# Kernel optimization log

Measured on AMD Instinct MI355X. Metric: run time of the kernel, lower is better.

Reference implementation:

```python
import jax, jax.numpy as jnp
import numpy as np

H = 8          # num heads
HD = 64        # head dim
DV = 512       # values_dim
DC = 128       # coords_dim
DI = 512       # att_inner_dim
DF = 2048      # mlp inner dim


def _ln(x, g, b, eps=1e-5):
    mu = jnp.mean(x, -1, keepdims=True)
    var = jnp.mean((x - mu) ** 2, -1, keepdims=True)
    return (x - mu) * jax.lax.rsqrt(var + eps) * g + b


def _rms(x, g, eps=1e-6):
    return x * jax.lax.rsqrt(jnp.mean(x * x, -1, keepdims=True) + eps) * g


def _heads(x):  # b n (h d) -> b h n d
    b, n, _ = x.shape
    return x.reshape(b, n, H, HD).transpose(0, 2, 1, 3)


def setup_inputs() -> dict:
    key = jax.random.key(0)
    ks = iter(jax.random.split(key, 40))
    r = lambda shape, s=0.02: jax.random.normal(next(ks), shape, jnp.float32) * s
    inp = {
        'coords': jax.random.normal(next(ks), (4, 4096, DC), jnp.float32),
        'values': jax.random.normal(next(ks), (4, 4096, DV), jnp.float32),
        'Lv': jax.random.normal(next(ks), (4, 1024, DV), jnp.float32),
        'Lc': jax.random.normal(next(ks), (4, 1024, DC), jnp.float32),
        'lam': jax.random.normal(next(ks), (1,), jnp.float32),
        'lvn_g': jnp.ones((DV,)), 'lvn_b': jnp.zeros((DV,)),
        'lcn_g': jnp.ones((DC,)), 'lcn_b': jnp.zeros((DC,)),
        'ck_w': r((DC, DI)), 'ck_b': jnp.zeros((DI,)), 'ck_g': jnp.ones((DI,)),
        'cq_w': r((DC, DI)), 'cq_b': jnp.zeros((DI,)), 'cq_g': jnp.ones((DI,)),
        'vq_w': r((DV, DI)), 'vq_b': jnp.zeros((DI,)), 'vq_g': jnp.ones((DI,)),
        'vk_w': r((DV, 2 * DI)), 'vk_b': jnp.zeros((2 * DI,)),
        'op_w': r((DI, DV)), 'op_b': jnp.zeros((DV,)),
        'oln_g': jnp.ones((DV,)), 'oln_b': jnp.zeros((DV,)),
        'm1_w': r((DV, DF)), 'm1_b': jnp.zeros((DF,)),
        'm2_w': r((DF, DF)), 'm2_b': jnp.zeros((DF,)),
        'm3_w': r((DF, DV)), 'm3_b': jnp.zeros((DV,)),
    }
    return inp


def reference(coords, values, Lv, Lc, lam, lvn_g, lvn_b, lcn_g, lcn_b,
              ck_w, ck_b, ck_g, cq_w, cq_b, cq_g, vq_w, vq_b, vq_g,
              vk_w, vk_b, op_w, op_b, oln_g, oln_b,
              m1_w, m1_b, m2_w, m2_b, m3_w, m3_b):
    Lv = _ln(Lv, lvn_g, lvn_b)
    Lc = _ln(Lc, lcn_g, lcn_b)
    vk = Lv @ vk_w + vk_b                     # [b, nl, 2*DI]
    v_v, k_v = jnp.split(vk, 2, axis=-1)
    k_c = _rms(Lc @ ck_w + ck_b, ck_g)
    k_c, v_v, k_v = _heads(k_c), _heads(v_v), _heads(k_v)  # [b,h,nl,d]
    q_v = _heads(_rms(values @ vq_w + vq_b, vq_g))         # [b,h,nq,d]
    q_c = _heads(_rms(coords @ cq_w + cq_b, cq_g))
    # dual-score attention
    scores = jnp.einsum('bhnd,bhmd->bhnm', q_c, k_c) \
        + lam[0] * jnp.einsum('bhnd,bhmd->bhnm', q_v, k_v)
    scores = scores / np.float32(np.sqrt(HD))
    attn = jax.nn.softmax(scores, axis=-1)
    V_out = jnp.einsum('bhnm,bhmd->bhnd', attn, v_v)       # [b,h,nq,d]
    b, _, nq, _ = V_out.shape
    V_out = V_out.transpose(0, 2, 1, 3).reshape(b, nq, DI)
    V_out = V_out @ op_w + op_b
    # (LayerNorm, MLP) head: Linear-GELU-Linear-GELU-Linear
    h = _ln(V_out, oln_g, oln_b)
    h = jax.nn.gelu(h @ m1_w + m1_b)
    h = jax.nn.gelu(h @ m2_w + m2_b)
    return h @ m3_w + m3_b
```

## Files before the change

### kernel.cpp

```cpp
#include <hip/hip_runtime.h>
#include <cstdint>
#include <cstddef>

typedef __bf16 bf16_t;
typedef __bf16 bf16x8 __attribute__((ext_vector_type(8)));
typedef __bf16 bf16x4 __attribute__((ext_vector_type(4)));
typedef float  f32x4  __attribute__((ext_vector_type(4)));

typedef __attribute__((address_space(1))) void gvoid_t;
typedef __attribute__((address_space(3))) void lvoid_t;

__device__ __forceinline__ f32x4 mfma16(bf16x8 a, bf16x8 b, f32x4 c) {
  return __builtin_amdgcn_mfma_f32_16x16x32_bf16(a, b, c, 0, 0, 0);
}

__device__ __forceinline__ void async_copy16(const void* g, void* l) {
  __builtin_amdgcn_global_load_lds((gvoid_t*)g, (lvoid_t*)l, 16, 0, 0);
}

__device__ __forceinline__ float gelu_tanh(float x) {
  float u = 0.7978845608028654f * (x + 0.044715f * x * x * x);
  float e = exp2f(2.8853900817779268f * u);
  float t = 1.f - 2.f / (e + 1.f);
  return 0.5f * x * (1.f + t);
}

struct TransBatch {
  const float* src[8];
  bf16_t* dst[8];
  int K[8], N[8], bx[8], base[8];
};

__global__ void transpose_batch_kernel(TransBatch d) {
  int id = blockIdx.x;
  int mi = 0;
#pragma unroll
  for (int j = 1; j < 8; j++)
    if (id >= d.base[j]) mi = j;
  int local = id - d.base[mi];
  int bxw = d.bx[mi];
  int n0 = (local % bxw) * 32, k0 = (local / bxw) * 32;
  const float* in = d.src[mi];
  bf16_t* out = d.dst[mi];
  int K = d.K[mi], N = d.N[mi];

  __shared__ float t[32][33];
  int tx = threadIdx.x, ty = threadIdx.y;
#pragma unroll
  for (int i = 0; i < 4; i++)
    t[ty + i * 8][tx] = in[(size_t)(k0 + ty + i * 8) * N + n0 + tx];
  __syncthreads();
#pragma unroll
  for (int i = 0; i < 4; i++)
    out[(size_t)(n0 + ty + i * 8) * K + k0 + tx] = (bf16_t)t[tx][ty + i * 8];
}

__global__ void transpose_v_kernel(const bf16_t* __restrict__ vk, bf16_t* __restrict__ vt) {
  __shared__ bf16_t t[32][33];
  int b = blockIdx.z;
  int d0 = blockIdx.x * 32, m0 = blockIdx.y * 32;
  int tx = threadIdx.x, ty = threadIdx.y;
#pragma unroll
  for (int i = 0; i < 4; i++)
    t[ty + i * 8][tx] = vk[((size_t)b * 1024 + m0 + ty + i * 8) * 1024 + d0 + tx];
  __syncthreads();
#pragma unroll
  for (int i = 0; i < 4; i++)
    vt[((size_t)b * 512 + d0 + ty + i * 8) * 1024 + m0 + tx] = t[tx][ty + i * 8];
}

__global__ void cvt2_bf16_kernel(const float* __restrict__ a, bf16_t* __restrict__ oa, int n4a,
                                 const float* __restrict__ b, bf16_t* __restrict__ ob, int n4b) {
  int i = blockIdx.x * blockDim.x + threadIdx.x;
  const float* s;
  bf16_t* o;
  int j;
  if (i < n4a) { s = a; o = oa; j = i; }
  else { j = i - n4a; if (j >= n4b) return; s = b; o = ob; }
  float4 v = ((const float4*)s)[j];
  bf16x4 r = {(bf16_t)v.x, (bf16_t)v.y, (bf16_t)v.z, (bf16_t)v.w};
  ((bf16x4*)o)[j] = r;
}

template <int D, typename TI>
__global__ void ln_kernel(const TI* __restrict__ x, const float* __restrict__ g,
                          const float* __restrict__ bb, bf16_t* __restrict__ out) {
  int row = blockIdx.x, t = threadIdx.x;
  float v = (float)x[(size_t)row * D + t];
  float s = v, s2 = v * v;
#pragma unroll
  for (int o = 32; o > 0; o >>= 1) { s += __shfl_xor(s, o); s2 += __shfl_xor(s2, o); }
  __shared__ float rs[8], rs2[8];
  constexpr int NW = D / 64;
  int w = t >> 6;
  if ((t & 63) == 0) { rs[w] = s; rs2[w] = s2; }
  __syncthreads();
  if (t < 64) {
    float a = (t < NW) ? rs[t] : 0.f;
    float a2 = (t < NW) ? rs2[t] : 0.f;
#pragma unroll
    for (int o = 4; o > 0; o >>= 1) { a += __shfl_xor(a, o); a2 += __shfl_xor(a2, o); }
    if (t == 0) { rs[0] = a; rs2[0] = a2; }
  }
  __syncthreads();
  float mu = rs[0] * (1.f / D);
  float var = rs2[0] * (1.f / D) - mu * mu;
  float rr = rsqrtf(var + 1e-5f);
  out[(size_t)row * D + t] = (bf16_t)((v - mu) * rr * g[t] + bb[t]);
}

template <typename TI>
__global__ void rms_kernel(const TI* __restrict__ x, const float* __restrict__ g,
                           bf16_t* __restrict__ out) {
  int row = blockIdx.x, t = threadIdx.x;
  float v = (float)x[(size_t)row * 512 + t];
  float s2 = v * v;
#pragma unroll
  for (int o = 32; o > 0; o >>= 1) s2 += __shfl_xor(s2, o);
  __shared__ float rs2[8];
  int w = t >> 6;
  if ((t & 63) == 0) rs2[w] = s2;
  __syncthreads();
  if (t < 64) {
    float a = (t < 8) ? rs2[t] : 0.f;
#pragma unroll
    for (int o = 4; o > 0; o >>= 1) a += __shfl_xor(a, o);
    if (t == 0) rs2[0] = a;
  }
  __syncthreads();
  float r = rsqrtf(rs2[0] * (1.f / 512.f) + 1e-6f);
  out[(size_t)row * 512 + t] = (bf16_t)(v * r * g[t]);
}

template <int EPI>
__global__ __launch_bounds__(256, 2) void gemm_bt(
    const bf16_t* __restrict__ A, const bf16_t* __restrict__ Bt,
    const float* __restrict__ bias, void* __restrict__ outp,
    int M, int N, int K) {
  __shared__ __align__(16) bf16_t As[128 * 64];
  __shared__ __align__(16) bf16_t Bs[128 * 64];
  const int tid = threadIdx.x;
  const int lane = tid & 63, wv = tid >> 6;
  const int quad = lane >> 4, l16 = lane & 15;
  const int m_base = blockIdx.y * 128, n_base = blockIdx.x * 128;
  const int wm = wv & 1, wn = wv >> 1;
  f32x4 acc[4][4] = {};

  for (int k0 = 0; k0 < K; k0 += 64) {
#pragma unroll
    for (int c = 0; c < 4; c++) {
      int p = c * 256 + tid;
      int row = p >> 3;
      int gc = (p & 7) ^ (row & 7);
      async_copy16(&A[(size_t)(m_base + row) * K + k0 + gc * 8], &As[(size_t)p * 8]);
      async_copy16(&Bt[(size_t)(n_base + row) * K + k0 + gc * 8], &Bs[(size_t)p * 8]);
    }
    __syncthreads();
#pragma unroll
    for (int ks = 0; ks < 2; ks++) {
      bf16x8 af[4], bfr[4];
#pragma unroll
      for (int mi = 0; mi < 4; mi++) {
        int r = wm * 64 + mi * 16 + l16;
        int c = (ks * 4 + quad) ^ (r & 7);
        af[mi] = *(const bf16x8*)&As[(size_t)(r * 8 + c) * 8];
      }
#pragma unroll
      for (int ni = 0; ni < 4; ni++) {
        int r = wn * 64 + ni * 16 + l16;
        int c = (ks * 4 + quad) ^ (r & 7);
        bfr[ni] = *(const bf16x8*)&Bs[(size_t)(r * 8 + c) * 8];
      }
#pragma unroll
      for (int mi = 0; mi < 4; mi++)
#pragma unroll
        for (int ni = 0; ni < 4; ni++)
          acc[mi][ni] = mfma16(af[mi], bfr[ni], acc[mi][ni]);
    }
    __syncthreads();
  }

#pragma unroll
  for (int mi = 0; mi < 4; mi++) {
    int m = m_base + wm * 64 + mi * 16 + quad * 4;
#pragma unroll
    for (int ni = 0; ni < 4; ni++) {
      int n = n_base + wn * 64 + ni * 16 + l16;
      float bv = bias[n];
#pragma unroll
      for (int r2 = 0; r2 < 4; r2++) {
        float v = acc[mi][ni][r2] + bv;
        if (EPI == 2) v = gelu_tanh(v);
        if (EPI == 0) ((float*)outp)[(size_t)(m + r2) * N + n] = v;
        else          ((bf16_t*)outp)[(size_t)(m + r2) * N + n] = (bf16_t)v;
      }
    }
  }
}

template <int EPI>
__global__ __launch_bounds__(256, 2) void gemm64(
    const bf16_t* __restrict__ A, const bf16_t* __restrict__ Bt,
    const float* __restrict__ bias, void* __restrict__ outp,
    int M, int N, int K) {
  __shared__ __align__(16) bf16_t As[64 * 32];
  __shared__ __align__(16) bf16_t Bs[128 * 32];
  const int tid = threadIdx.x;
  const int lane = tid & 63, wv = tid >> 6;
  const int quad = lane >> 4, l16 = lane & 15;
  const int m_base = blockIdx.y * 64, n_base = blockIdx.x * 128;
  const int wm = wv & 1, wn = wv >> 1;
  f32x4 acc[2][4] = {};

  for (int k0 = 0; k0 < K; k0 += 32) {
    {
      int p = tid;
      int row = p >> 2;
      int kc = (p & 3) ^ ((row >> 1) & 3);
      async_copy16(&A[(size_t)(m_base + row) * K + k0 + kc * 8], &As[(size_t)p * 8]);
    }
#pragma unroll
    for (int c = 0; c < 2; c++) {
      int p = c * 256 + tid;
      int row = p >> 2;
      int kc = (p & 3) ^ ((row >> 1) & 3);
      async_copy16(&Bt[(size_t)(n_base + row) * K + k0 + kc * 8], &Bs[(size_t)p * 8]);
    }
    __syncthreads();
    bf16x8 af[2], bfr[4];
#pragma unroll
    for (int mi = 0; mi < 2; mi++) {
      int r = wm * 32 + mi * 16 + l16;
      int kc = quad ^ ((r >> 1) & 3);
      af[mi] = *(const bf16x8*)&As[(size_t)(r * 4 + kc) * 8];
    }
#pragma unroll
    for (int ni = 0; ni < 4; ni++) {
      int r = wn * 64 + ni * 16 + l16;
      int kc = quad ^ ((r >> 1) & 3);
      bfr[ni] = *(const bf16x8*)&Bs[(size_t)(r * 4 + kc) * 8];
    }
#pragma unroll
    for (int mi = 0; mi < 2; mi++)
#pragma unroll
      for (int ni = 0; ni < 4; ni++)
        acc[mi][ni] = mfma16(af[mi], bfr[ni], acc[mi][ni]);
    __syncthreads();
  }

#pragma unroll
  for (int mi = 0; mi < 2; mi++) {
    int m = m_base + wm * 32 + mi * 16 + quad * 4;
#pragma unroll
    for (int ni = 0; ni < 4; ni++) {
      int n = n_base + wn * 64 + ni * 16 + l16;
      float bv = bias[n];
#pragma unroll
      for (int r2 = 0; r2 < 4; r2++) {
        float v = acc[mi][ni][r2] + bv;
        if (EPI == 2) v = gelu_tanh(v);
        if (EPI == 0) ((float*)outp)[(size_t)(m + r2) * N + n] = v;
        else          ((bf16_t*)outp)[(size_t)(m + r2) * N + n] = (bf16_t)v;
      }
    }
  }
}

__global__ __launch_bounds__(256, 2) void attn_kernel(
    const bf16_t* __restrict__ qc, const bf16_t* __restrict__ qv,
    const bf16_t* __restrict__ kcb, const bf16_t* __restrict__ vkb,
    const bf16_t* __restrict__ vt, const float* __restrict__ lamp,
    bf16_t* __restrict__ vout) {
  const int b = blockIdx.z, h = blockIdx.y;
  const int tid = threadIdx.x;
  const int lane = tid & 63, wv = tid >> 6;
  const int quad = lane >> 4, l16 = lane & 15;
  const int qrow0 = blockIdx.x * 128 + wv * 32;
  const float SCL = 0.125f * 1.4426950408889634f;
  const float C1 = SCL, C2 = lamp[0] * SCL;

  __shared__ __align__(16) bf16_t kcS[64 * 64];
  __shared__ __align__(16) bf16_t kvS[64 * 64];
  __shared__ __align__(16) bf16_t vtS[64 * 64];
  __shared__ __align__(16) bf16_t sP[4][32 * 64];
  bf16_t* sPw = sP[wv];

  bf16x8 qcf[2][2], qvf[2][2];
#pragma unroll
  for (int mt = 0; mt < 2; mt++)
#pragma unroll
    for (int ks = 0; ks < 2; ks++) {
      size_t o = ((size_t)b * 4096 + qrow0 + mt * 16 + l16) * 512 + h * 64 + ks * 32 + quad * 8;
      qcf[mt][ks] = *(const bf16x8*)&qc[o];
      qvf[mt][ks] = *(const bf16x8*)&qv[o];
    }

  f32x4 O[2][4] = {};
  float ls[2][4] = {};

  for (int kb = 0; kb < 16; kb++) {
#pragma unroll
    for (int i = 0; i < 2; i++) {
      int p = i * 256 + tid;
      int row = p >> 3;
      int gc = (p & 7) ^ (row & 7);
      async_copy16(&kcb[((size_t)b * 1024 + kb * 64 + row) * 512 + h * 64 + gc * 8],
                   &kcS[(size_t)p * 8]);
      async_copy16(&vkb[((size_t)b * 1024 + kb * 64 + row) * 1024 + 512 + h * 64 + gc * 8],
                   &kvS[(size_t)p * 8]);
      async_copy16(&vt[((size_t)((b * 8 + h) * 64) + row) * 1024 + kb * 64 + gc * 8],
                   &vtS[(size_t)p * 8]);
    }
    __syncthreads();

#pragma unroll
    for (int nt = 0; nt < 4; nt++) {
      int krow = nt * 16 + l16;
      int kb8 = krow & 7;
      bf16x8 kc0 = *(const bf16x8*)&kcS[(size_t)(krow * 8 + (quad ^ kb8)) * 8];
      bf16x8 kc1 = *(const bf16x8*)&kcS[(size_t)(krow * 8 + ((4 + quad) ^ kb8)) * 8];
      bf16x8 kv0 = *(const bf16x8*)&kvS[(size_t)(krow * 8 + (quad ^ kb8)) * 8];
      bf16x8 kv1 = *(const bf16x8*)&kvS[(size_t)(krow * 8 + ((4 + quad) ^ kb8)) * 8];
#pragma unroll
      for (int mt = 0; mt < 2; mt++) {
        f32x4 sc = {};
        sc = mfma16(qcf[mt][0], kc0, sc);
        sc = mfma16(qcf[mt][1], kc1, sc);
        f32x4 sv = {};
        sv = mfma16(qvf[mt][0], kv0, sv);
        sv = mfma16(qvf[mt][1], kv1, sv);
#pragma unroll
        for (int r = 0; r < 4; r++) {
          float p = exp2f(sc[r] * C1 + sv[r] * C2);
          ls[mt][r] += p;
          int prow = mt * 16 + quad * 4 + r;
          int col = nt * 16 + l16;
          sPw[prow * 64 + (((col >> 3) ^ (prow & 7)) * 8) + (col & 7)] = (bf16_t)p;
        }
      }
    }
    asm volatile("s_waitcnt lgkmcnt(0)" ::: "memory");

#pragma unroll
    for (int ks2 = 0; ks2 < 2; ks2++) {
      bf16x8 pa[2];
#pragma unroll
      for (int mt = 0; mt < 2; mt++) {
        int prow = mt * 16 + l16;
        pa[mt] = *(const bf16x8*)&sPw[(size_t)(prow * 8 + ((ks2 * 4 + quad) ^ (prow & 7))) * 8];
      }
#pragma unroll
      for (int ntd = 0; ntd < 4; ntd++) {
        int drow = ntd * 16 + l16;
        bf16x8 vb = *(const bf16x8*)&vtS[(size_t)(drow * 8 + ((ks2 * 4 + quad) ^ (drow & 7))) * 8];
        O[0][ntd] = mfma16(pa[0], vb, O[0][ntd]);
        O[1][ntd] = mfma16(pa[1], vb, O[1][ntd]);
      }
    }
    __syncthreads();
  }

#pragma unroll
  for (int mt = 0; mt < 2; mt++) {
    float inv[4];
#pragma unroll
    for (int r = 0; r < 4; r++) {
      float v = ls[mt][r];
      v += __shfl_xor(v, 1);
      v += __shfl_xor(v, 2);
      v += __shfl_xor(v, 4);
      v += __shfl_xor(v, 8);
      inv[r] = 1.f / v;
    }
#pragma unroll
    for (int ntd = 0; ntd < 4; ntd++)
#pragma unroll
      for (int r = 0; r < 4; r++) {
        size_t o = ((size_t)b * 4096 + qrow0 + mt * 16 + quad * 4 + r) * 512 + h * 64 + ntd * 16 + l16;
        vout[o] = (bf16_t)(O[mt][ntd][r] * inv[r]);
      }
  }
}

extern "C" void kernel_launch(void* const* d_in, const int* in_sizes, int n_in,
                              void* d_out, int out_size, void* d_ws, size_t ws_size,
                              hipStream_t stream) {
  (void)in_sizes; (void)n_in; (void)out_size; (void)ws_size;
  const float* coords = (const float*)d_in[0];
  const float* values = (const float*)d_in[1];
  const float* Lv     = (const float*)d_in[2];
  const float* Lc     = (const float*)d_in[3];
  const float* lam    = (const float*)d_in[4];
  const float* lvn_g  = (const float*)d_in[5];
  const float* lvn_b  = (const float*)d_in[6];
  const float* lcn_g  = (const float*)d_in[7];
  const float* lcn_b  = (const float*)d_in[8];
  const float* ck_w = (const float*)d_in[9];  const float* ck_b = (const float*)d_in[10]; const float* ck_g = (const float*)d_in[11];
  const float* cq_w = (const float*)d_in[12]; const float* cq_b = (const float*)d_in[13]; const float* cq_g = (const float*)d_in[14];
  const float* vq_w = (const float*)d_in[15]; const float* vq_b = (const float*)d_in[16]; const float* vq_g = (const float*)d_in[17];
  const float* vk_w = (const float*)d_in[18]; const float* vk_b = (const float*)d_in[19];
  const float* op_w = (const float*)d_in[20]; const float* op_b = (const float*)d_in[21];
  const float* oln_g = (const float*)d_in[22]; const float* oln_b = (const float*)d_in[23];
  const float* m1_w = (const float*)d_in[24]; const float* m1_b = (const float*)d_in[25];
  const float* m2_w = (const float*)d_in[26]; const float* m2_b = (const float*)d_in[27];
  const float* m3_w = (const float*)d_in[28]; const float* m3_b = (const float*)d_in[29];

  char* ws = (char*)d_ws;
  size_t off = 0;
  auto alloc = [&](size_t bytes) { void* p = ws + off; off += (bytes + 255) & ~(size_t)255; return p; };

  bf16_t* wt_m1 = (bf16_t*)alloc((size_t)512 * 2048 * 2);
  bf16_t* wt_m2 = (bf16_t*)alloc((size_t)2048 * 2048 * 2);
  bf16_t* wt_m3 = (bf16_t*)alloc((size_t)2048 * 512 * 2);
  bf16_t* scr0  = (bf16_t*)alloc((size_t)16384 * 512 * 4);
  bf16_t* qv_bf = (bf16_t*)alloc((size_t)16384 * 512 * 2);
  bf16_t* qc_bf = (bf16_t*)alloc((size_t)16384 * 512 * 2);
  bf16_t* voutb = (bf16_t*)alloc((size_t)16384 * 512 * 2);
  bf16_t* h0    = (bf16_t*)alloc((size_t)16384 * 512 * 2);
  bf16_t* h1    = (bf16_t*)alloc((size_t)16384 * 2048 * 2);
  bf16_t* h2    = (bf16_t*)alloc((size_t)16384 * 2048 * 2);

  size_t ov = (size_t)((char*)h1 - ws);
  auto oalloc = [&](size_t bytes) { void* p = ws + ov; ov += (bytes + 255) & ~(size_t)255; return p; };
  bf16_t* wt_vk = (bf16_t*)oalloc((size_t)1024 * 512 * 2);
  bf16_t* wt_ck = (bf16_t*)oalloc((size_t)512 * 128 * 2);
  bf16_t* wt_cq = (bf16_t*)oalloc((size_t)512 * 128 * 2);
  bf16_t* wt_vq = (bf16_t*)oalloc((size_t)512 * 512 * 2);
  bf16_t* wt_op = (bf16_t*)oalloc((size_t)512 * 512 * 2);
  bf16_t* lv_ln = (bf16_t*)oalloc((size_t)4096 * 512 * 2);
  bf16_t* lc_ln = (bf16_t*)oalloc((size_t)4096 * 128 * 2);
  bf16_t* vkob  = (bf16_t*)oalloc((size_t)4096 * 1024 * 2);
  bf16_t* kc_b  = (bf16_t*)oalloc((size_t)4096 * 512 * 2);
  bf16_t* kc_bf = (bf16_t*)oalloc((size_t)4096 * 512 * 2);
  bf16_t* val_bf= (bf16_t*)oalloc((size_t)16384 * 512 * 2);
  bf16_t* crd_bf= (bf16_t*)oalloc((size_t)16384 * 128 * 2);
  bf16_t* vt    = (bf16_t*)oalloc((size_t)4 * 512 * 1024 * 2);

  TransBatch tb8;
  const float* srcs[8] = {vk_w, ck_w, cq_w, vq_w, op_w, m1_w, m2_w, m3_w};
  bf16_t* dsts[8] = {wt_vk, wt_ck, wt_cq, wt_vq, wt_op, wt_m1, wt_m2, wt_m3};
  int Ks[8] = {512, 128, 128, 512, 512, 512, 2048, 2048};
  int Ns[8] = {1024, 512, 512, 512, 512, 2048, 2048, 512};
  int cum = 0;
  for (int i = 0; i < 8; i++) {
    tb8.src[i] = srcs[i]; tb8.dst[i] = dsts[i];
    tb8.K[i] = Ks[i]; tb8.N[i] = Ns[i];
    tb8.bx[i] = Ns[i] / 32;
    tb8.base[i] = cum;
    cum += (Ns[i] / 32) * (Ks[i] / 32);
  }
  transpose_batch_kernel<<<cum, dim3(32, 8), 0, stream>>>(tb8);

  cvt2_bf16_kernel<<<(16384 * 512 / 4 + 16384 * 128 / 4 + 255) / 256, 256, 0, stream>>>(
      values, val_bf, 16384 * 512 / 4, coords, crd_bf, 16384 * 128 / 4);

  ln_kernel<512, float><<<4096, 512, 0, stream>>>(Lv, lvn_g, lvn_b, lv_ln);
  ln_kernel<128, float><<<4096, 128, 0, stream>>>(Lc, lcn_g, lcn_b, lc_ln);

  gemm64<1><<<dim3(8, 64), 256, 0, stream>>>(lv_ln, wt_vk, vk_b, vkob, 4096, 1024, 512);
  gemm64<1><<<dim3(4, 64), 256, 0, stream>>>(lc_ln, wt_ck, ck_b, kc_b, 4096, 512, 128);
  rms_kernel<bf16_t><<<4096, 512, 0, stream>>>(kc_b, ck_g, kc_bf);

  gemm64<1><<<dim3(4, 256), 256, 0, stream>>>(val_bf, wt_vq, vq_b, scr0, 16384, 512, 512);
  rms_kernel<bf16_t><<<16384, 512, 0, stream>>>(scr0, vq_g, qv_bf);
  gemm64<1><<<dim3(4, 256), 256, 0, stream>>>(crd_bf, wt_cq, cq_b, scr0, 16384, 512, 128);
  rms_kernel<bf16_t><<<16384, 512, 0, stream>>>(scr0, cq_g, qc_bf);

  transpose_v_kernel<<<dim3(16, 32, 4), dim3(32, 8), 0, stream>>>(vkob, vt);

  attn_kernel<<<dim3(32, 8, 4), 256, 0, stream>>>(qc_bf, qv_bf, kc_bf, vkob, vt, lam, voutb);

  gemm64<1><<<dim3(4, 256), 256, 0, stream>>>(voutb, wt_op, op_b, scr0, 16384, 512, 512);
  ln_kernel<512, bf16_t><<<16384, 512, 0, stream>>>(scr0, oln_g, oln_b, h0);

  gemm_bt<2><<<dim3(16, 128), 256, 0, stream>>>(h0, wt_m1, m1_b, h1, 16384, 2048, 512);
  gemm_bt<2><<<dim3(16, 128), 256, 0, stream>>>(h1, wt_m2, m2_b, h2, 16384, 2048, 2048);
  gemm_bt<0><<<dim3(4, 128), 256, 0, stream>>>(h2, wt_m3, m3_b, (float*)d_out, 16384, 512, 2048);
}
```

Measured before the change: 688.9 us.

## Add pipelined 256x256 GEMM for MLP, wave-per-row norms, XCD block remap

Adds a 512-thread 256x256-tile GEMM with double-buffered LDS, async global-to-LDS loads interleaved with MFMA phases, explicit barriers and s_setprio. It is used for the two large MLP GEMMs to raise data reuse and overlap loads with math. LayerNorm and RMSNorm are merged into one wave-per-row kernel with vector loads and no shared-memory reduction. The existing 128-tile GEMM also gets an XCD-aware block index remap for cache locality. The hand-tuned vmcnt waits and the 128 KB of LDS are fragile and may limit occupancy.

```diff
diff --git a/kernel.cpp b/kernel.cpp
--- a/kernel.cpp
+++ b/kernel.cpp
@@ -5,6 +5,7 @@
 typedef __bf16 bf16_t;
 typedef __bf16 bf16x8 __attribute__((ext_vector_type(8)));
 typedef __bf16 bf16x4 __attribute__((ext_vector_type(4)));
+typedef __bf16 bf16x2 __attribute__((ext_vector_type(2)));
 typedef float  f32x4  __attribute__((ext_vector_type(4)));
 
 typedef __attribute__((address_space(1))) void gvoid_t;
@@ -82,54 +83,59 @@
   ((bf16x4*)o)[j] = r;
 }
 
-template <int D, typename TI>
-__global__ void ln_kernel(const TI* __restrict__ x, const float* __restrict__ g,
-                          const float* __restrict__ bb, bf16_t* __restrict__ out) {
-  int row = blockIdx.x, t = threadIdx.x;
-  float v = (float)x[(size_t)row * D + t];
-  float s = v, s2 = v * v;
+template <int D, bool IS_RMS, typename TI>
+__global__ __launch_bounds__(256) void rownorm_kernel(
+    const TI* __restrict__ x, const float* __restrict__ g,
+    const float* __restrict__ bb, bf16_t* __restrict__ out) {
+  constexpr int V = D / 64;
+  const int row = blockIdx.x * 4 + (threadIdx.x >> 6);
+  const int lane = threadIdx.x & 63;
+  const size_t base = (size_t)row * D + (size_t)lane * V;
+  float v[V];
+  if constexpr (sizeof(TI) == 2) {
+    bf16x8 xv = *(const bf16x8*)(x + base);
+#pragma unroll
+    for (int j = 0; j < V; j++) v[j] = (float)xv[j];
+  } else if constexpr (V == 8) {
+    float4 a = ((const float4*)(x + base))[0];
+    float4 b2 = ((const float4*)(x + base))[1];
+    v[0] = a.x; v[1] = a.y; v[2] = a.z; v[3] = a.w;
+    v[4] = b2.x; v[5] = b2.y; v[6] = b2.z; v[7] = b2.w;
+  } else {
+    float2 a = *(const float2*)(x + base);
+    v[0] = a.x; v[1] = a.y;
+  }
+  float s = 0.f, s2 = 0.f;
+#pragma unroll
+  for (int j = 0; j < V; j++) { s += v[j]; s2 += v[j] * v[j]; }
 #pragma unroll
   for (int o = 32; o > 0; o >>= 1) { s += __shfl_xor(s, o); s2 += __shfl_xor(s2, o); }
-  __shared__ float rs[8], rs2[8];
-  constexpr int NW = D / 64;
-  int w = t >> 6;
-  if ((t & 63) == 0) { rs[w] = s; rs2[w] = s2; }
-  __syncthreads();
-  if (t < 64) {
-    float a = (t < NW) ? rs[t] : 0.f;
-    float a2 = (t < NW) ? rs2[t] : 0.f;
-#pragma unroll
-    for (int o = 4; o > 0; o >>= 1) { a += __shfl_xor(a, o); a2 += __shfl_xor(a2, o); }
-    if (t == 0) { rs[0] = a; rs2[0] = a2; }
-  }
-  __syncthreads();
-  float mu = rs[0] * (1.f / D);
-  float var = rs2[0] * (1.f / D) - mu * mu;
-  float rr = rsqrtf(var + 1e-5f);
-  out[(size_t)row * D + t] = (bf16_t)((v - mu) * rr * g[t] + bb[t]);
-}
-
-template <typename TI>
-__global__ void rms_kernel(const TI* __restrict__ x, const float* __restrict__ g,
-                           bf16_t* __restrict__ out) {
-  int row = blockIdx.x, t = threadIdx.x;
-  float v = (float)x[(size_t)row * 512 + t];
-  float s2 = v * v;
-#pragma unroll
-  for (int o = 32; o > 0; o >>= 1) s2 += __shfl_xor(s2, o);
-  __shared__ float rs2[8];
-  int w = t >> 6;
-  if ((t & 63) == 0) rs2[w] = s2;
-  __syncthreads();
-  if (t < 64) {
-    float a = (t < 8) ? rs2[t] : 0.f;
-#pragma unroll
-    for (int o = 4; o > 0; o >>= 1) a += __shfl_xor(a, o);
-    if (t == 0) rs2[0] = a;
-  }
-  __syncthreads();
-  float r = rsqrtf(rs2[0] * (1.f / 512.f) + 1e-6f);
-  out[(size_t)row * 512 + t] = (bf16_t)(v * r * g[t]);
+  float mu, rr;
+  if constexpr (IS_RMS) {
+    mu = 0.f;
+    rr = rsqrtf(s2 * (1.f / D) + 1e-6f);
+  } else {
+    mu = s * (1.f / D);
+    rr = rsqrtf(s2 * (1.f / D) - mu * mu + 1e-5f);
+  }
+  float o[V];
+#pragma unroll
+  for (int j = 0; j < V; j++) {
+    float gv = g[lane * V + j];
+    float bv;
+    if constexpr (IS_RMS) bv = 0.f; else bv = bb[lane * V + j];
+    o[j] = (v[j] - mu) * rr * gv + bv;
+  }
+  if constexpr (V == 8) {
+    bf16x8 ov;
+#pragma unroll
+    for (int j = 0; j < 8; j++) ov[j] = (bf16_t)o[j];
+    *(bf16x8*)(out + base) = ov;
+  } else {
+    bf16x2 ov;
+    ov[0] = (bf16_t)o[0]; ov[1] = (bf16_t)o[1];
+    *(bf16x2*)(out + base) = ov;
+  }
 }
 
 template <int EPI>
@@ -142,7 +148,10 @@
   const int tid = threadIdx.x;
   const int lane = tid & 63, wv = tid >> 6;
   const int quad = lane >> 4, l16 = lane & 15;
-  const int m_base = blockIdx.y * 128, n_base = blockIdx.x * 128;
+  int nwg = gridDim.x * gridDim.y;
+  int bid = blockIdx.y * gridDim.x + blockIdx.x;
+  if (!(nwg & 7)) { int cpx = nwg >> 3; bid = (bid & 7) * cpx + (bid >> 3); }
+  const int m_base = (bid / gridDim.x) * 128, n_base = (bid % gridDim.x) * 128;
   const int wm = wv & 1, wn = wv >> 1;
   f32x4 acc[4][4] = {};
 
@@ -190,6 +199,144 @@
 #pragma unroll
       for (int r2 = 0; r2 < 4; r2++) {
         float v = acc[mi][ni][r2] + bv;
+        if (EPI == 2) v = gelu_tanh(v);
+        if (EPI == 0) ((float*)outp)[(size_t)(m + r2) * N + n] = v;
+        else          ((bf16_t*)outp)[(size_t)(m + r2) * N + n] = (bf16_t)v;
+      }
+    }
+  }
+}
+
+#define PH_TAIL(...) \
+  __builtin_amdgcn_s_barrier(); \
+  asm volatile("s_waitcnt lgkmcnt(0)" ::: "memory"); \
+  __builtin_amdgcn_s_setprio(1); \
+  __VA_ARGS__; \
+  __builtin_amdgcn_s_setprio(0); \
+  __builtin_amdgcn_s_barrier();
+
+#define PH_TAIL_VM(...) \
+  asm volatile("s_waitcnt vmcnt(6)" ::: "memory"); \
+  PH_TAIL(__VA_ARGS__)
+
+template <int EPI>
+__global__ __launch_bounds__(512, 2) void gemm256(
+    const bf16_t* __restrict__ A, const bf16_t* __restrict__ Bt,
+    const float* __restrict__ bias, void* __restrict__ outp,
+    int M, int N, int K) {
+  __shared__ __align__(16) bf16_t As[2][256 * 64];
+  __shared__ __align__(16) bf16_t Bs[2][256 * 64];
+  const int tid = threadIdx.x;
+  const int lane = tid & 63, wid = tid >> 6;
+  const int quad = lane >> 4, l16 = lane & 15;
+  const int wm = wid >> 2, wn = wid & 3;
+  int nwg = gridDim.x * gridDim.y;
+  int bid = blockIdx.y * gridDim.x + blockIdx.x;
+  if (!(nwg & 7)) { int cpx = nwg >> 3; bid = (bid & 7) * cpx + (bid >> 3); }
+  const int m_base = (bid / gridDim.x) * 256, n_base = (bid % gridDim.x) * 256;
+  const int nkt = K >> 6, nit = nkt >> 1;
+
+  f32x4 acc[8][4] = {};
+
+  auto stA = [&](int buf, int half, int kt) {
+    if (kt >= nkt) kt = 0;
+    const bf16_t* src = A + (size_t)(m_base + half * 128) * K + kt * 64;
+    bf16_t* dst = &As[buf][half * 128 * 64];
+#pragma unroll
+    for (int i = 0; i < 2; i++) {
+      int p = i * 512 + tid;
+      int r = p >> 3, pc = p & 7;
+      int gc = pc ^ (r & 7);
+      async_copy16(&src[(size_t)r * K + gc * 8], &dst[(size_t)p * 8]);
+    }
+  };
+  auto stB = [&](int buf, int half, int kt) {
+    if (kt >= nkt) kt = 0;
+    const bf16_t* src = Bt + (size_t)(n_base + half * 128) * K + kt * 64;
+    bf16_t* dst = &Bs[buf][half * 128 * 64];
+#pragma unroll
+    for (int i = 0; i < 2; i++) {
+      int p = i * 512 + tid;
+      int r = p >> 3, pc = p & 7;
+      int gc = pc ^ (r & 7);
+      async_copy16(&src[(size_t)r * K + gc * 8], &dst[(size_t)p * 8]);
+    }
+  };
+  auto ldA = [&](const bf16_t* Asb, int rg, bf16x8 (&af)[2][2]) {
+#pragma unroll
+    for (int mi = 0; mi < 2; mi++) {
+      int r = wm * 128 + rg * 32 + mi * 16 + l16;
+#pragma unroll
+      for (int ks = 0; ks < 2; ks++) {
+        int c = (ks * 4 + quad) ^ (r & 7);
+        af[mi][ks] = *(const bf16x8*)&Asb[(size_t)(r * 8 + c) * 8];
+      }
+    }
+  };
+  auto ldB = [&](const bf16_t* Bsb, bf16x8 (&bfr)[4][2]) {
+#pragma unroll
+    for (int cf = 0; cf < 4; cf++) {
+      int r = wn * 64 + cf * 16 + l16;
+#pragma unroll
+      for (int ks = 0; ks < 2; ks++) {
+        int c = (ks * 4 + quad) ^ (r & 7);
+        bfr[cf][ks] = *(const bf16x8*)&Bsb[(size_t)(r * 8 + c) * 8];
+      }
+    }
+  };
+  auto mm = [&](int rg, bf16x8 (&a)[2][2], bf16x8 (&b)[4][2]) {
+#pragma unroll
+    for (int ks = 0; ks < 2; ks++)
+#pragma unroll
+      for (int mi = 0; mi < 2; mi++)
+#pragma unroll
+        for (int cf = 0; cf < 4; cf++)
+          acc[rg * 2 + mi][cf] = mfma16(a[mi][ks], b[cf][ks], acc[rg * 2 + mi][cf]);
+  };
+
+  stB(0, 0, 0); stB(0, 1, 0); stA(0, 0, 0); stA(0, 1, 0);
+  stB(1, 0, 1); stB(1, 1, 1); stA(1, 0, 1);
+  asm volatile("s_waitcnt vmcnt(6)" ::: "memory");
+  __builtin_amdgcn_s_barrier();
+
+  bf16x8 af[2][2], afn[2][2], bfr[4][2];
+  for (int it = 0; it < nit; ++it) {
+    const int O = 2 * it + 1, F = 2 * it + 2, G = 2 * it + 3;
+    ldB(Bs[0], bfr); ldA(As[0], 0, af);
+    stA(1, 1, O);
+    PH_TAIL(mm(0, af, bfr));
+    ldA(As[0], 1, af);
+    stB(0, 0, F);
+    PH_TAIL(mm(1, af, bfr));
+    ldA(As[0], 2, af); ldA(As[0], 3, afn);
+    stB(0, 1, F);
+    PH_TAIL(mm(2, af, bfr));
+    stA(0, 0, F);
+    PH_TAIL_VM(mm(3, afn, bfr));
+    ldB(Bs[1], bfr); ldA(As[1], 0, af);
+    stA(0, 1, F);
+    PH_TAIL(mm(0, af, bfr));
+    ldA(As[1], 1, af);
+    stB(1, 0, G);
+    PH_TAIL(mm(1, af, bfr));
+    ldA(As[1], 2, af); ldA(As[1], 3, afn);
+    stB(1, 1, G);
+    PH_TAIL(mm(2, af, bfr));
+    stA(1, 0, G);
+    PH_TAIL_VM(mm(3, afn, bfr));
+  }
+  asm volatile("s_waitcnt vmcnt(0)" ::: "memory");
+
+#pragma unroll
+  for (int rf = 0; rf < 8; rf++) {
+    int m = m_base + wm * 128 + rf * 16 + quad * 4;
+#pragma unroll
+    for (int cf = 0; cf < 4; cf++) {
+      int n = n_base + wn * 64 + cf * 16 + l16;
+      float bv = bias[n];
+#pragma unroll
+      for (int r2 = 0; r2 < 4; r2++) {
+        float v = acc[rf][cf][r2] + bv;
         if (EPI == 2) v = gelu_tanh(v);
         if (EPI == 0) ((float*)outp)[(size_t)(m + r2) * N + n] = v;
         else          ((bf16_t*)outp)[(size_t)(m + r2) * N + n] = (bf16_t)v;
@@ -454,26 +601,26 @@
   cvt2_bf16_kernel<<<(16384 * 512 / 4 + 16384 * 128 / 4 + 255) / 256, 256, 0, stream>>>(
       values, val_bf, 16384 * 512 / 4, coords, crd_bf, 16384 * 128 / 4);
 
-  ln_kernel<512, float><<<4096, 512, 0, stream>>>(Lv, lvn_g, lvn_b, lv_ln);
-  ln_kernel<128, float><<<4096, 128, 0, stream>>>(Lc, lcn_g, lcn_b, lc_ln);
+  rownorm_kernel<512, false, float><<<1024, 256, 0, stream>>>(Lv, lvn_g, lvn_b, lv_ln);
+  rownorm_kernel<128, false, float><<<1024, 256, 0, stream>>>(Lc, lcn_g, lcn_b, lc_ln);
 
   gemm64<1><<<dim3(8, 64), 256, 0, stream>>>(lv_ln, wt_vk, vk_b, vkob, 4096, 1024, 512);
   gemm64<1><<<dim3(4, 64), 256, 0, stream>>>(lc_ln, wt_ck, ck_b, kc_b, 4096, 512, 128);
-  rms_kernel<bf16_t><<<4096, 512, 0, stream>>>(kc_b, ck_g, kc_bf);
+  rownorm_kernel<512, true, bf16_t><<<1024, 256, 0, stream>>>(kc_b, ck_g, nullptr, kc_bf);
 
   gemm64<1><<<dim3(4, 256), 256, 0, stream>>>(val_bf, wt_vq, vq_b, scr0, 16384, 512, 512);
-  rms_kernel<bf16_t><<<16384, 512, 0, stream>>>(scr0, vq_g, qv_bf);
+  rownorm_kernel<512, true, bf16_t><<<4096, 256, 0, stream>>>(scr0, vq_g, nullptr, qv_bf);
   gemm64<1><<<dim3(4, 256), 256, 0, stream>>>(crd_bf, wt_cq, cq_b, scr0, 16384, 512, 128);
-  rms_kernel<bf16_t><<<16384, 512, 0, stream>>>(scr0, cq_g, qc_bf);
+  rownorm_kernel<512, true, bf16_t><<<4096, 256, 0, stream>>>(scr0, cq_g, nullptr, qc_bf);
 
   transpose_v_kernel<<<dim3(16, 32, 4), dim3(32, 8), 0, stream>>>(vkob, vt);
 
   attn_kernel<<<dim3(32, 8, 4), 256, 0, stream>>>(qc_bf, qv_bf, kc_bf, vkob, vt, lam, voutb);
 
   gemm64<1><<<dim3(4, 256), 256, 0, stream>>>(voutb, wt_op, op_b, scr0, 16384, 512, 512);
-  ln_kernel<512, bf16_t><<<16384, 512, 0, stream>>>(scr0, oln_g, oln_b, h0);
-
-  gemm_bt<2><<<dim3(16, 128), 256, 0, stream>>>(h0, wt_m1, m1_b, h1, 16384, 2048, 512);
-  gemm_bt<2><<<dim3(16, 128), 256, 0, stream>>>(h1, wt_m2, m2_b, h2, 16384, 2048, 2048);
+  rownorm_kernel<512, false, bf16_t><<<4096, 256, 0, stream>>>(scr0, oln_g, oln_b, h0);
+
+  gemm256<2><<<dim3(8, 64), 512, 0, stream>>>(h0, wt_m1, m1_b, h1, 16384, 2048, 512);
+  gemm256<2><<<dim3(8, 64), 512, 0, stream>>>(h1, wt_m2, m2_b, h2, 16384, 2048, 2048);
   gemm_bt<0><<<dim3(4, 128), 256, 0, stream>>>(h2, wt_m3, m3_b, (float*)d_out, 16384, 512, 2048);
 }
```

Measured after the change: 611.7 us. 1.13x faster.
